# Kernel tuning notes

Measured on AMD Instinct MI355X. Metric: run time of the kernel, lower is better.

Reference implementation:

```python
import jax, jax.numpy as jnp
import numpy as np

B, D, L, G, K, U, OUT = 131072, 256, 3, 4, 128, 64, 10


def setup_inputs() -> dict:
    key = jax.random.key(0)
    k1, k2, k3, k4 = jax.random.split(key, 4)
    x = jax.random.normal(k1, (B, D), dtype=jnp.float32)
    # per-level, per-group input node coords into the previous level's output
    idx = jax.random.randint(k2, (L, G, K), 0, D, dtype=jnp.int32)
    # per-group kernels [fan_in, units] and biases [units], stacked
    W = jax.random.normal(k3, (L, G, K, U), dtype=jnp.float32) * 0.1
    b = jnp.zeros((L, G, U), dtype=jnp.float32)
    W_out = jax.random.normal(k4, (D, OUT), dtype=jnp.float32) * 0.1
    b_out = jnp.zeros((OUT,), dtype=jnp.float32)
    return {"x": x, "idx": idx, "W": W, "b": b, "W_out": W_out, "b_out": b_out}


def reference(x, idx, W, b, W_out, b_out):
    # Each topological level: for every dependency-group g, gather K scalar
    # columns from the previous level (the per-node slice+concat in the
    # original), tiny matmul [B,K]@[K,U] + bias, tanh; level output is the
    # concat of group outputs -> [B, G*U]. Groups share shapes, so they are
    # batched over axis g with a single einsum per level.
    h = x
    n_levels = W.shape[0]
    for l in range(n_levels):  # small fixed loop over topology levels
        gathered = h[:, idx[l]]                                  # [B, G, K]
        z = jnp.einsum('bgk,gku->bgu', gathered, W[l]) + b[l]    # [B, G, U]
        h = jnp.tanh(z).reshape(z.shape[0], -1)                  # [B, G*U]
    # output level: single group fed by all previous nodes, linear out activation
    return h @ W_out + b_out                                      # [B, OUT]
```

## Files before the change

kernel.cpp:

```cpp
#include <hip/hip_runtime.h>

typedef unsigned short ushort_t;
typedef __attribute__((ext_vector_type(8))) short short8;
typedef __attribute__((ext_vector_type(4))) float floatx4;

#define DD 256
#define LL 3
#define GG 4
#define KK 128
#define UU 64
#define OUTN 10
#define HSTRIDE 264
#define MROWS 128

__device__ __forceinline__ ushort_t f2bf(float f) {
  unsigned u = __builtin_bit_cast(unsigned, f);
  u = (u + 0x7FFFu + ((u >> 16) & 1u)) >> 16;
  return (ushort_t)u;
}

__device__ __forceinline__ unsigned pack_bf2(float lo, float hi) {
  unsigned a = __builtin_bit_cast(unsigned, hi) + 0x8000u;
  unsigned b = __builtin_bit_cast(unsigned, lo) + 0x8000u;
  return __builtin_amdgcn_perm(a, b, 0x07060302u);
}

__device__ __forceinline__ float fast_tanh(float x) {
  float e = __builtin_amdgcn_exp2f(x * 2.885390081777927f);
  return __builtin_fmaf(-2.0f, __builtin_amdgcn_rcpf(e + 1.0f), 1.0f);
}

__global__ __launch_bounds__(256) void prep_kernel(
    const int* __restrict__ idx, const float* __restrict__ W,
    const float* __restrict__ Wout, ushort_t* __restrict__ AT,
    ushort_t* __restrict__ WoT) {
  int b = blockIdx.x;
  int t = threadIdx.x;
  if (b < LL * DD) {
    int l = b >> 8, n = b & 255, g = n >> 6, u = n & 63;
    __shared__ int sidx[KK];
    __shared__ float sw[KK];
    if (t < KK) {
      sidx[t] = idx[(l * GG + g) * KK + t];
      sw[t]   = W[((size_t)((l * GG + g) * KK + t)) * UU + u];
    }
    __syncthreads();
    float s = 0.f;
#pragma unroll 8
    for (int j = 0; j < KK; j++) s += (sidx[j] == t) ? sw[j] : 0.f;
    AT[(b << 8) | t] = f2bf(s);
  } else {
    int e2 = (b - LL * DD) * 256 + t;
    int n = e2 >> 8, k = e2 & 255;
    WoT[e2] = (n < OUTN) ? f2bf(Wout[k * OUTN + n]) : (ushort_t)0;
  }
}

__global__ __launch_bounds__(256, 2) void fused_kernel(
    const float* __restrict__ x, const float* __restrict__ bias,
    const float* __restrict__ bout, const ushort_t* __restrict__ AT,
    const ushort_t* __restrict__ WoT, float* __restrict__ out) {
  __shared__ ushort_t hbuf[MROWS * HSTRIDE];

  const int tid  = threadIdx.x;
  const int wave = tid >> 6;
  const int lane = tid & 63;
  const int quad = lane >> 4;
  const int l16  = lane & 15;
  const long row0 = (long)blockIdx.x * MROWS;

  const float4* xv = (const float4*)(x + row0 * DD);
#pragma unroll
  for (int i = 0; i < 32; i++) {
    int f  = tid + i * 256;
    int r  = f >> 6;
    int c4 = f & 63;
    float4 v = xv[r * 64 + c4];
    uint2 w;
    w.x = pack_bf2(v.x, v.y);
    w.y = pack_bf2(v.z, v.w);
    *(uint2*)&hbuf[r * HSTRIDE + c4 * 4] = w;
  }
  __syncthreads();

#pragma unroll 1
  for (int l = 0; l < 3; l++) {
    const ushort_t* Ab   = AT + l * (DD * DD) + (wave * 64 + l16) * DD + quad * 8;
    const ushort_t* hsrc = hbuf + l16 * HSTRIDE + quad * 8;

    floatx4 acc[8][4];
#pragma unroll
    for (int nt = 0; nt < 4; nt++) {
      float4 bv = *(const float4*)&bias[l * DD + wave * 64 + nt * 16 + quad * 4];
      floatx4 ini = {bv.x, bv.y, bv.z, bv.w};
#pragma unroll
      for (int mt = 0; mt < 8; mt++) acc[mt][nt] = ini;
    }

    short8 wf[4], wfn[4];
#pragma unroll
    for (int nt = 0; nt < 4; nt++) wf[nt] = *(const short8*)&Ab[nt * 16 * DD];

#pragma unroll
    for (int ks = 0; ks < 8; ks++) {
      if (ks < 7) {
#pragma unroll
        for (int nt = 0; nt < 4; nt++)
          wfn[nt] = *(const short8*)&Ab[nt * 16 * DD + (ks + 1) * 32];
      }
      short8 bfc = *(const short8*)&hsrc[0 * 16 * HSTRIDE + ks * 32];
#pragma unroll
      for (int mt = 0; mt < 8; mt++) {
        short8 bfn;
        if (mt < 7) bfn = *(const short8*)&hsrc[(mt + 1) * 16 * HSTRIDE + ks * 32];
        acc[mt][0] = __builtin_amdgcn_mfma_f32_16x16x32_bf16(wf[0], bfc, acc[mt][0], 0, 0, 0);
        acc[mt][1] = __builtin_amdgcn_mfma_f32_16x16x32_bf16(wf[1], bfc, acc[mt][1], 0, 0, 0);
        acc[mt][2] = __builtin_amdgcn_mfma_f32_16x16x32_bf16(wf[2], bfc, acc[mt][2], 0, 0, 0);
        acc[mt][3] = __builtin_amdgcn_mfma_f32_16x16x32_bf16(wf[3], bfc, acc[mt][3], 0, 0, 0);
        bfc = bfn;
      }
#pragma unroll
      for (int nt = 0; nt < 4; nt++) wf[nt] = wfn[nt];
    }
    __syncthreads();

#pragma unroll
    for (int mt = 0; mt < 8; mt++) {
#pragma unroll
      for (int nt = 0; nt < 4; nt++) {
        uint2 w;
        w.x = pack_bf2(fast_tanh(acc[mt][nt][0]), fast_tanh(acc[mt][nt][1]));
        w.y = pack_bf2(fast_tanh(acc[mt][nt][2]), fast_tanh(acc[mt][nt][3]));
        *(uint2*)&hbuf[(mt * 16 + l16) * HSTRIDE + wave * 64 + nt * 16 + quad * 4] = w;
      }
    }
    __syncthreads();
  }

  short8 wof[8];
#pragma unroll
  for (int ks = 0; ks < 8; ks++)
    wof[ks] = *(const short8*)&WoT[l16 * DD + ks * 32 + quad * 8];

#pragma unroll
  for (int c = 0; c < 2; c++) {
    const int mrow = wave * 32 + c * 16 + l16;
    floatx4 accf = {0.f, 0.f, 0.f, 0.f};
#pragma unroll
    for (int ks = 0; ks < 8; ks++) {
      short8 bfr = *(const short8*)&hbuf[mrow * HSTRIDE + ks * 32 + quad * 8];
      accf = __builtin_amdgcn_mfma_f32_16x16x32_bf16(wof[ks], bfr, accf, 0, 0, 0);
    }
    const long obase = (row0 + mrow) * OUTN;
    if (quad < 2) {
      float4 p = {accf[0] + bout[quad * 4 + 0], accf[1] + bout[quad * 4 + 1],
                  accf[2] + bout[quad * 4 + 2], accf[3] + bout[quad * 4 + 3]};
      *(float4*)&out[obase + quad * 4] = p;
    } else if (quad == 2) {
      float2 p = {accf[0] + bout[8], accf[1] + bout[9]};
      *(float2*)&out[obase + 8] = p;
    }
  }
}

extern "C" void kernel_launch(void* const* d_in, const int* in_sizes, int n_in,
                              void* d_out, int out_size, void* d_ws, size_t ws_size,
                              hipStream_t stream) {
  const float* x    = (const float*)d_in[0];
  const int*   idx  = (const int*)d_in[1];
  const float* W    = (const float*)d_in[2];
  const float* b    = (const float*)d_in[3];
  const float* Wout = (const float*)d_in[4];
  const float* bout = (const float*)d_in[5];
  float* out = (float*)d_out;

  ushort_t* AT  = (ushort_t*)d_ws;
  ushort_t* WoT = AT + LL * DD * DD;

  prep_kernel<<<LL * DD + 16, 256, 0, stream>>>(idx, W, Wout, AT, WoT);
  fused_kernel<<<131072 / MROWS, 256, 0, stream>>>(x, b, bout, AT, WoT, out);
}
```

Baseline: 271.5 us.

## Halve rows per block, raise occupancy, double-buffer fragments with explicit MFMA scheduling

Cuts the rows each block handles from 128 to 64, which halves the shared-memory tile and accumulator registers and allows three blocks per CU instead of two. The k-loop now double-buffers both the weight and activation fragments a full step ahead and uses sched_group_barrier to interleave the loads with the 16 MFMAs. The price is twice as many blocks, each reloading the dense weight matrix, so more weight traffic per row and less reuse of each weight fragment.

```diff
diff --git a/kernel.cpp b/kernel.cpp
--- a/kernel.cpp
+++ b/kernel.cpp
@@ -11,7 +11,7 @@
 #define UU 64
 #define OUTN 10
 #define HSTRIDE 264
-#define MROWS 128
+#define MROWS 64
 
 __device__ __forceinline__ ushort_t f2bf(float f) {
   unsigned u = __builtin_bit_cast(unsigned, f);
@@ -56,7 +56,7 @@
   }
 }
 
-__global__ __launch_bounds__(256, 2) void fused_kernel(
+__global__ __launch_bounds__(256, 3) void fused_kernel(
     const float* __restrict__ x, const float* __restrict__ bias,
     const float* __restrict__ bout, const ushort_t* __restrict__ AT,
     const ushort_t* __restrict__ WoT, float* __restrict__ out) {
@@ -71,7 +71,7 @@
 
   const float4* xv = (const float4*)(x + row0 * DD);
 #pragma unroll
-  for (int i = 0; i < 32; i++) {
+  for (int i = 0; i < 16; i++) {
     int f  = tid + i * 256;
     int r  = f >> 6;
     int c4 = f & 63;
@@ -83,49 +83,52 @@
   }
   __syncthreads();
 
+  const ushort_t* hsrc = hbuf + l16 * HSTRIDE + quad * 8;
+
 #pragma unroll 1
   for (int l = 0; l < 3; l++) {
-    const ushort_t* Ab   = AT + l * (DD * DD) + (wave * 64 + l16) * DD + quad * 8;
-    const ushort_t* hsrc = hbuf + l16 * HSTRIDE + quad * 8;
+    const ushort_t* Ab = AT + l * (DD * DD) + (wave * 64 + l16) * DD + quad * 8;
 
-    floatx4 acc[8][4];
+    floatx4 acc[4][4];
 #pragma unroll
     for (int nt = 0; nt < 4; nt++) {
       float4 bv = *(const float4*)&bias[l * DD + wave * 64 + nt * 16 + quad * 4];
       floatx4 ini = {bv.x, bv.y, bv.z, bv.w};
 #pragma unroll
-      for (int mt = 0; mt < 8; mt++) acc[mt][nt] = ini;
+      for (int mt = 0; mt < 4; mt++) acc[mt][nt] = ini;
     }
 
-    short8 wf[4], wfn[4];
+    short8 a[2][4], b[2][4];
 #pragma unroll
-    for (int nt = 0; nt < 4; nt++) wf[nt] = *(const short8*)&Ab[nt * 16 * DD];
+    for (int nt = 0; nt < 4; nt++) a[0][nt] = *(const short8*)&Ab[nt * 16 * DD];
+#pragma unroll
+    for (int mt = 0; mt < 4; mt++) b[0][mt] = *(const short8*)&hsrc[mt * 16 * HSTRIDE];
 
 #pragma unroll
     for (int ks = 0; ks < 8; ks++) {
-      if (ks < 7) {
+      const int cur = ks & 1, nxt = cur ^ 1;
+      const int kn = ((ks + 1) & 7) * 32;
+#pragma unroll
+      for (int mt = 0; mt < 4; mt++)
+        b[nxt][mt] = *(const short8*)&hsrc[mt * 16 * HSTRIDE + kn];
+#pragma unroll
+      for (int nt = 0; nt < 4; nt++)
+        a[nxt][nt] = *(const short8*)&Ab[nt * 16 * DD + kn];
+#pragma unroll
+      for (int mt = 0; mt < 4; mt++) {
 #pragma unroll
         for (int nt = 0; nt < 4; nt++)
-          wfn[nt] = *(const short8*)&Ab[nt * 16 * DD + (ks + 1) * 32];
+          acc[mt][nt] = __builtin_amdgcn_mfma_f32_16x16x32_bf16(
+              a[cur][nt], b[cur][mt], acc[mt][nt], 0, 0, 0);
       }
-      short8 bfc = *(const short8*)&hsrc[0 * 16 * HSTRIDE + ks * 32];
-#pragma unroll
-      for (int mt = 0; mt < 8; mt++) {
-        short8 bfn;
-        if (mt < 7) bfn = *(const short8*)&hsrc[(mt + 1) * 16 * HSTRIDE + ks * 32];
-        acc[mt][0] = __builtin_amdgcn_mfma_f32_16x16x32_bf16(wf[0], bfc, acc[mt][0], 0, 0, 0);
-        acc[mt][1] = __builtin_amdgcn_mfma_f32_16x16x32_bf16(wf[1], bfc, acc[mt][1], 0, 0, 0);
-        acc[mt][2] = __builtin_amdgcn_mfma_f32_16x16x32_bf16(wf[2], bfc, acc[mt][2], 0, 0, 0);
-        acc[mt][3] = __builtin_amdgcn_mfma_f32_16x16x32_bf16(wf[3], bfc, acc[mt][3], 0, 0, 0);
-        bfc = bfn;
-      }
-#pragma unroll
-      for (int nt = 0; nt < 4; nt++) wf[nt] = wfn[nt];
+      __builtin_amdgcn_sched_group_barrier(0x100, 4, 0);
+      __builtin_amdgcn_sched_group_barrier(0x020, 4, 0);
+      __builtin_amdgcn_sched_group_barrier(0x008, 16, 0);
     }
     __syncthreads();
 
 #pragma unroll
-    for (int mt = 0; mt < 8; mt++) {
+    for (int mt = 0; mt < 4; mt++) {
 #pragma unroll
       for (int nt = 0; nt < 4; nt++) {
         uint2 w;
@@ -142,24 +145,20 @@
   for (int ks = 0; ks < 8; ks++)
     wof[ks] = *(const short8*)&WoT[l16 * DD + ks * 32 + quad * 8];
 
+  floatx4 accf = {0.f, 0.f, 0.f, 0.f};
 #pragma unroll
-  for (int c = 0; c < 2; c++) {
-    const int mrow = wave * 32 + c * 16 + l16;
-    floatx4 accf = {0.f, 0.f, 0.f, 0.f};
-#pragma unroll
-    for (int ks = 0; ks < 8; ks++) {
-      short8 bfr = *(const short8*)&hbuf[mrow * HSTRIDE + ks * 32 + quad * 8];
-      accf = __builtin_amdgcn_mfma_f32_16x16x32_bf16(wof[ks], bfr, accf, 0, 0, 0);
-    }
-    const long obase = (row0 + mrow) * OUTN;
-    if (quad < 2) {
-      float4 p = {accf[0] + bout[quad * 4 + 0], accf[1] + bout[quad * 4 + 1],
-                  accf[2] + bout[quad * 4 + 2], accf[3] + bout[quad * 4 + 3]};
-      *(float4*)&out[obase + quad * 4] = p;
-    } else if (quad == 2) {
-      float2 p = {accf[0] + bout[8], accf[1] + bout[9]};
-      *(float2*)&out[obase + 8] = p;
-    }
+  for (int ks = 0; ks < 8; ks++) {
+    short8 bfr = *(const short8*)&hbuf[(wave * 16 + l16) * HSTRIDE + ks * 32 + quad * 8];
+    accf = __builtin_amdgcn_mfma_f32_16x16x32_bf16(wof[ks], bfr, accf, 0, 0, 0);
+  }
+  const long obase = (row0 + wave * 16 + l16) * OUTN;
+  if (quad < 2) {
+    float4 p = {accf[0] + bout[quad * 4 + 0], accf[1] + bout[quad * 4 + 1],
+                accf[2] + bout[quad * 4 + 2], accf[3] + bout[quad * 4 + 3]};
+    *(float4*)&out[obase + quad * 4] = p;
+  } else if (quad == 2) {
+    float2 p = {accf[0] + bout[8], accf[1] + bout[9]};
+    *(float2*)&out[obase + 8] = p;
   }
 }
 
```

New measurement: 304.1 us. +12.0%, slower.
